# Kernel tuning notes

Measured on AMD Instinct MI355X. Metric: run time of the kernel, lower is better.

Reference implementation:

```python
import jax, jax.numpy as jnp
import numpy as np

B, IN_DIM, OUT_DIM = 4096, 8192, 8192

# Each of the 16 gates op_i(a,b) is affine in (1, a, b, a*b).
# Rows: [const, coef_a, coef_b, coef_ab] for gate i = 0..15.
GATE_COEF = np.array([
    [0.,  0.,  0.,  0.],   # 0: zeros
    [0.,  0.,  0.,  1.],   # 1: a*b
    [0.,  1.,  0., -1.],   # 2: a - a*b
    [0.,  1.,  0.,  0.],   # 3: a
    [0.,  0.,  1., -1.],   # 4: b - a*b
    [0.,  0.,  1.,  0.],   # 5: b
    [0.,  1.,  1., -2.],   # 6: a + b - 2ab (xor)
    [0.,  1.,  1., -1.],   # 7: a + b - ab (or)
    [1., -1., -1.,  1.],   # 8: 1 - (a + b - ab)
    [1., -1., -1.,  2.],   # 9: 1 - (a + b - 2ab)
    [1.,  0., -1.,  0.],   # 10: 1 - b
    [1.,  0., -1.,  1.],   # 11: 1 - b + ab
    [1., -1.,  0.,  0.],   # 12: 1 - a
    [1., -1.,  0.,  1.],   # 13: 1 - a + ab
    [1.,  0.,  0., -1.],   # 14: 1 - ab
    [1.,  0.,  0.,  0.],   # 15: ones
], dtype=np.float32)


def setup_inputs() -> dict:
    key = jax.random.key(0)
    k1, k2, k3, k4 = jax.random.split(key, 4)
    x = jax.random.uniform(k1, (B, IN_DIM), dtype=jnp.float32)
    weights = jax.random.normal(k2, (OUT_DIM, 16), dtype=jnp.float32)
    idx0 = jax.random.randint(k3, (OUT_DIM,), 0, IN_DIM)
    idx1 = jax.random.randint(k4, (OUT_DIM,), 0, IN_DIM)
    return {"x": x, "weights": weights, "idx0": idx0, "idx1": idx1}


def reference(x, weights, idx0, idx1):
    # training path: soft mixture over 16 gates
    p = jax.nn.softmax(weights, axis=-1)          # [out_dim, 16]
    c = p @ jnp.asarray(GATE_COEF)                # [out_dim, 4]: sum_i p_i * op_i collapsed
    a = x[:, idx0]                                # [B, out_dim]
    b = x[:, idx1]                                # [B, out_dim]
    return c[:, 0] + c[:, 1] * a + c[:, 2] * b + c[:, 3] * (a * b)
```

## Files before the change

kernel.cpp:

```cpp
#include <hip/hip_runtime.h>

#define IN_DIM 8192
#define OUT_DIM 8192
#define NROWS 4096
#define THREADS 1024
#define GRID 256
#define RPB (NROWS / GRID)
#define JG (OUT_DIM / (THREADS * 4))

static_assert(GRID * RPB == NROWS, "row partition");
static_assert(JG * THREADS * 4 == OUT_DIM, "col partition");

typedef float v4f __attribute__((ext_vector_type(4)));

#define BLOCK_SYNC_LDS()                                   \
  do {                                                     \
    asm volatile("s_waitcnt lgkmcnt(0)" ::: "memory");     \
    __builtin_amdgcn_s_barrier();                          \
    asm volatile("" ::: "memory");                         \
  } while (0)

static __device__ __forceinline__ void softmax_c(const float* __restrict__ w, int jbase,
                                                 v4f* C0, v4f* C1, v4f* C2, v4f* C3) {
  static constexpr float G[16][4] = {
      {0.f, 0.f, 0.f, 0.f}, {0.f, 0.f, 0.f, 1.f}, {0.f, 1.f, 0.f, -1.f}, {0.f, 1.f, 0.f, 0.f},
      {0.f, 0.f, 1.f, -1.f}, {0.f, 0.f, 1.f, 0.f}, {0.f, 1.f, 1.f, -2.f}, {0.f, 1.f, 1.f, -1.f},
      {1.f, -1.f, -1.f, 1.f}, {1.f, -1.f, -1.f, 2.f}, {1.f, 0.f, -1.f, 0.f}, {1.f, 0.f, -1.f, 1.f},
      {1.f, -1.f, 0.f, 0.f}, {1.f, -1.f, 0.f, 1.f}, {1.f, 0.f, 0.f, -1.f}, {1.f, 0.f, 0.f, 0.f}};
#pragma unroll
  for (int q = 0; q < 4; ++q) {
    const float4* wp = (const float4*)(w + (size_t)(jbase + q) * 16);
    float4 w0 = wp[0], w1 = wp[1], w2 = wp[2], w3 = wp[3];
    float wa[16] = {w0.x, w0.y, w0.z, w0.w, w1.x, w1.y, w1.z, w1.w,
                    w2.x, w2.y, w2.z, w2.w, w3.x, w3.y, w3.z, w3.w};
    float m = wa[0];
#pragma unroll
    for (int k = 1; k < 16; ++k) m = fmaxf(m, wa[k]);
    float s = 0.f;
    float p[16];
#pragma unroll
    for (int k = 0; k < 16; ++k) { p[k] = __expf(wa[k] - m); s += p[k]; }
    const float inv = 1.f / s;
    float a0 = 0.f, a1 = 0.f, a2 = 0.f, a3 = 0.f;
#pragma unroll
    for (int k = 0; k < 16; ++k) {
      a0 = fmaf(p[k], G[k][0], a0);
      a1 = fmaf(p[k], G[k][1], a1);
      a2 = fmaf(p[k], G[k][2], a2);
      a3 = fmaf(p[k], G[k][3], a3);
    }
    (*C0)[q] = a0 * inv; (*C1)[q] = a1 * inv; (*C2)[q] = a2 * inv; (*C3)[q] = a3 * inv;
  }
}

__global__ __launch_bounds__(THREADS, 4) void gate_fused(
    const float* __restrict__ x, const float* __restrict__ w,
    const int* __restrict__ idx0, const int* __restrict__ idx1,
    float* __restrict__ out) {
  __shared__ __align__(16) float buf[2][IN_DIM];
  const int tid = threadIdx.x;
  const int r0 = blockIdx.x * RPB;

  int4 i0[JG], i1[JG];
  v4f C0[JG], C1[JG], C2[JG], C3[JG];
#pragma unroll
  for (int g = 0; g < JG; ++g) {
    const int j = tid * 4 + g * (THREADS * 4);
    i0[g] = *(const int4*)(idx0 + j);
    i1[g] = *(const int4*)(idx1 + j);
    softmax_c(w, j, &C0[g], &C1[g], &C2[g], &C3[g]);
  }

  v4f ra[2];
  const float* x0 = x + (size_t)r0 * IN_DIM;
#pragma unroll
  for (int t = 0; t < 2; ++t) ra[t] = __builtin_nontemporal_load((const v4f*)x0 + tid + t * THREADS);
#pragma unroll
  for (int t = 0; t < 2; ++t) ((v4f*)buf[0])[tid + t * THREADS] = ra[t];
#pragma unroll
  for (int t = 0; t < 2; ++t)
    ra[t] = __builtin_nontemporal_load((const v4f*)(x0 + IN_DIM) + tid + t * THREADS);
  BLOCK_SYNC_LDS();

#pragma unroll 1
  for (int p = 0; p < RPB; ++p) {
    if (p + 1 < RPB) {
      v4f* dst = (v4f*)buf[(p + 1) & 1];
#pragma unroll
      for (int t = 0; t < 2; ++t) dst[tid + t * THREADS] = ra[t];
    }
    if (p + 2 < RPB) {
      const float* xs = x + (size_t)(r0 + p + 2) * IN_DIM;
#pragma unroll
      for (int t = 0; t < 2; ++t)
        ra[t] = __builtin_nontemporal_load((const v4f*)xs + tid + t * THREADS);
    }
    const float* bufc = buf[p & 1];
    float* o = out + (size_t)(r0 + p) * OUT_DIM;
#pragma unroll
    for (int g = 0; g < JG; ++g) {
      const int4 ia = i0[g], ib = i1[g];
      v4f a, b;
      a.x = bufc[ia.x]; a.y = bufc[ia.y]; a.z = bufc[ia.z]; a.w = bufc[ia.w];
      b.x = bufc[ib.x]; b.y = bufc[ib.y]; b.z = bufc[ib.z]; b.w = bufc[ib.w];
      const v4f r = C0[g] + C1[g] * a + C2[g] * b + C3[g] * (a * b);
      __builtin_nontemporal_store(r, (v4f*)(o + tid * 4 + g * (THREADS * 4)));
    }
    BLOCK_SYNC_LDS();
  }
}

extern "C" void kernel_launch(void* const* d_in, const int* in_sizes, int n_in,
                              void* d_out, int out_size, void* d_ws, size_t ws_size,
                              hipStream_t stream) {
  const float* x = (const float*)d_in[0];
  const float* weights = (const float*)d_in[1];
  const int* idx0 = (const int*)d_in[2];
  const int* idx1 = (const int*)d_in[3];
  float* out = (float*)d_out;
  gate_fused<<<GRID, THREADS, 0, stream>>>(x, weights, idx0, idx1, out);
}
```

Before: 246.6 us.

## Precompute gate coefficients in separate kernel and halve block size

Moves the softmax-to-coefficient computation into a small preceding kernel that writes the four coefficient arrays to workspace. The main kernel now reloads those coefficients from global memory on every row instead of holding them in registers. Blocks shrink to 512 threads and the grid doubles to 512, so each block handles fewer rows with its double-buffered LDS staging. This aims to remove redundant per-block softmax work and raise occupancy, at the cost of an extra launch and repeated coefficient loads from cache.

```diff
diff --git a/kernel.cpp b/kernel.cpp
--- a/kernel.cpp
+++ b/kernel.cpp
@@ -3,13 +3,15 @@
 #define IN_DIM 8192
 #define OUT_DIM 8192
 #define NROWS 4096
-#define THREADS 1024
-#define GRID 256
+#define THREADS 512
+#define GRID 512
 #define RPB (NROWS / GRID)
 #define JG (OUT_DIM / (THREADS * 4))
+#define SV (IN_DIM / (THREADS * 4))
 
 static_assert(GRID * RPB == NROWS, "row partition");
 static_assert(JG * THREADS * 4 == OUT_DIM, "col partition");
+static_assert(SV * THREADS * 4 == IN_DIM, "stage partition");
 
 typedef float v4f __attribute__((ext_vector_type(4)));
 
@@ -20,41 +22,47 @@
     asm volatile("" ::: "memory");                         \
   } while (0)
 
-static __device__ __forceinline__ void softmax_c(const float* __restrict__ w, int jbase,
-                                                 v4f* C0, v4f* C1, v4f* C2, v4f* C3) {
-  static constexpr float G[16][4] = {
-      {0.f, 0.f, 0.f, 0.f}, {0.f, 0.f, 0.f, 1.f}, {0.f, 1.f, 0.f, -1.f}, {0.f, 1.f, 0.f, 0.f},
-      {0.f, 0.f, 1.f, -1.f}, {0.f, 0.f, 1.f, 0.f}, {0.f, 1.f, 1.f, -2.f}, {0.f, 1.f, 1.f, -1.f},
-      {1.f, -1.f, -1.f, 1.f}, {1.f, -1.f, -1.f, 2.f}, {1.f, 0.f, -1.f, 0.f}, {1.f, 0.f, -1.f, 1.f},
-      {1.f, -1.f, 0.f, 0.f}, {1.f, -1.f, 0.f, 1.f}, {1.f, 0.f, 0.f, -1.f}, {1.f, 0.f, 0.f, 0.f}};
+__device__ __constant__ float GATE_COEF[16][4] = {
+    {0.f, 0.f, 0.f, 0.f}, {0.f, 0.f, 0.f, 1.f}, {0.f, 1.f, 0.f, -1.f}, {0.f, 1.f, 0.f, 0.f},
+    {0.f, 0.f, 1.f, -1.f}, {0.f, 0.f, 1.f, 0.f}, {0.f, 1.f, 1.f, -2.f}, {0.f, 1.f, 1.f, -1.f},
+    {1.f, -1.f, -1.f, 1.f}, {1.f, -1.f, -1.f, 2.f}, {1.f, 0.f, -1.f, 0.f}, {1.f, 0.f, -1.f, 1.f},
+    {1.f, -1.f, 0.f, 0.f}, {1.f, -1.f, 0.f, 1.f}, {1.f, 0.f, 0.f, -1.f}, {1.f, 0.f, 0.f, 0.f}};
+
+__global__ __launch_bounds__(256) void compute_c_kernel(const float* __restrict__ w,
+                                                        float* __restrict__ cp) {
+  int j = blockIdx.x * blockDim.x + threadIdx.x;
+  if (j >= OUT_DIM) return;
+  const float4* wv = (const float4*)(w + (size_t)j * 16);
+  float4 w0 = wv[0], w1 = wv[1], w2 = wv[2], w3 = wv[3];
+  float wa[16] = {w0.x, w0.y, w0.z, w0.w, w1.x, w1.y, w1.z, w1.w,
+                  w2.x, w2.y, w2.z, w2.w, w3.x, w3.y, w3.z, w3.w};
+  float m = wa[0];
 #pragma unroll
-  for (int q = 0; q < 4; ++q) {
-    const float4* wp = (const float4*)(w + (size_t)(jbase + q) * 16);
-    float4 w0 = wp[0], w1 = wp[1], w2 = wp[2], w3 = wp[3];
-    float wa[16] = {w0.x, w0.y, w0.z, w0.w, w1.x, w1.y, w1.z, w1.w,
-                    w2.x, w2.y, w2.z, w2.w, w3.x, w3.y, w3.z, w3.w};
-    float m = wa[0];
+  for (int k = 1; k < 16; ++k) m = fmaxf(m, wa[k]);
+  float p[16];
+  float s = 0.f;
 #pragma unroll
-    for (int k = 1; k < 16; ++k) m = fmaxf(m, wa[k]);
-    float s = 0.f;
-    float p[16];
+  for (int k = 0; k < 16; ++k) {
+    p[k] = __expf(wa[k] - m);
+    s += p[k];
+  }
+  float inv = 1.f / s;
+  float c0 = 0.f, c1 = 0.f, c2 = 0.f, c3 = 0.f;
 #pragma unroll
-    for (int k = 0; k < 16; ++k) { p[k] = __expf(wa[k] - m); s += p[k]; }
-    const float inv = 1.f / s;
-    float a0 = 0.f, a1 = 0.f, a2 = 0.f, a3 = 0.f;
-#pragma unroll
-    for (int k = 0; k < 16; ++k) {
-      a0 = fmaf(p[k], G[k][0], a0);
-      a1 = fmaf(p[k], G[k][1], a1);
-      a2 = fmaf(p[k], G[k][2], a2);
-      a3 = fmaf(p[k], G[k][3], a3);
-    }
-    (*C0)[q] = a0 * inv; (*C1)[q] = a1 * inv; (*C2)[q] = a2 * inv; (*C3)[q] = a3 * inv;
+  for (int k = 0; k < 16; ++k) {
+    c0 = fmaf(p[k], GATE_COEF[k][0], c0);
+    c1 = fmaf(p[k], GATE_COEF[k][1], c1);
+    c2 = fmaf(p[k], GATE_COEF[k][2], c2);
+    c3 = fmaf(p[k], GATE_COEF[k][3], c3);
   }
+  cp[j] = c0 * inv;
+  cp[j + OUT_DIM] = c1 * inv;
+  cp[j + 2 * OUT_DIM] = c2 * inv;
+  cp[j + 3 * OUT_DIM] = c3 * inv;
 }
 
-__global__ __launch_bounds__(THREADS, 4) void gate_fused(
-    const float* __restrict__ x, const float* __restrict__ w,
+__global__ __launch_bounds__(THREADS, 4) void gate_persist(
+    const float* __restrict__ x, const float* __restrict__ cp,
     const int* __restrict__ idx0, const int* __restrict__ idx1,
     float* __restrict__ out) {
   __shared__ __align__(16) float buf[2][IN_DIM];
@@ -62,23 +70,27 @@
   const int r0 = blockIdx.x * RPB;
 
   int4 i0[JG], i1[JG];
-  v4f C0[JG], C1[JG], C2[JG], C3[JG];
 #pragma unroll
   for (int g = 0; g < JG; ++g) {
     const int j = tid * 4 + g * (THREADS * 4);
     i0[g] = *(const int4*)(idx0 + j);
     i1[g] = *(const int4*)(idx1 + j);
-    softmax_c(w, j, &C0[g], &C1[g], &C2[g], &C3[g]);
   }
 
-  v4f ra[2];
+  const float* c0p = cp;
+  const float* c1p = cp + OUT_DIM;
+  const float* c2p = cp + 2 * OUT_DIM;
+  const float* c3p = cp + 3 * OUT_DIM;
+
+  v4f ra[SV];
   const float* x0 = x + (size_t)r0 * IN_DIM;
 #pragma unroll
-  for (int t = 0; t < 2; ++t) ra[t] = __builtin_nontemporal_load((const v4f*)x0 + tid + t * THREADS);
+  for (int t = 0; t < SV; ++t)
+    ra[t] = __builtin_nontemporal_load((const v4f*)x0 + tid + t * THREADS);
 #pragma unroll
-  for (int t = 0; t < 2; ++t) ((v4f*)buf[0])[tid + t * THREADS] = ra[t];
+  for (int t = 0; t < SV; ++t) ((v4f*)buf[0])[tid + t * THREADS] = ra[t];
 #pragma unroll
-  for (int t = 0; t < 2; ++t)
+  for (int t = 0; t < SV; ++t)
     ra[t] = __builtin_nontemporal_load((const v4f*)(x0 + IN_DIM) + tid + t * THREADS);
   BLOCK_SYNC_LDS();
 
@@ -87,24 +99,29 @@
     if (p + 1 < RPB) {
       v4f* dst = (v4f*)buf[(p + 1) & 1];
 #pragma unroll
-      for (int t = 0; t < 2; ++t) dst[tid + t * THREADS] = ra[t];
+      for (int t = 0; t < SV; ++t) dst[tid + t * THREADS] = ra[t];
     }
     if (p + 2 < RPB) {
       const float* xs = x + (size_t)(r0 + p + 2) * IN_DIM;
 #pragma unroll
-      for (int t = 0; t < 2; ++t)
+      for (int t = 0; t < SV; ++t)
         ra[t] = __builtin_nontemporal_load((const v4f*)xs + tid + t * THREADS);
     }
     const float* bufc = buf[p & 1];
     float* o = out + (size_t)(r0 + p) * OUT_DIM;
 #pragma unroll
     for (int g = 0; g < JG; ++g) {
+      const int j = tid * 4 + g * (THREADS * 4);
+      const v4f c0v = *(const v4f*)(c0p + j);
+      const v4f c1v = *(const v4f*)(c1p + j);
+      const v4f c2v = *(const v4f*)(c2p + j);
+      const v4f c3v = *(const v4f*)(c3p + j);
       const int4 ia = i0[g], ib = i1[g];
       v4f a, b;
       a.x = bufc[ia.x]; a.y = bufc[ia.y]; a.z = bufc[ia.z]; a.w = bufc[ia.w];
       b.x = bufc[ib.x]; b.y = bufc[ib.y]; b.z = bufc[ib.z]; b.w = bufc[ib.w];
-      const v4f r = C0[g] + C1[g] * a + C2[g] * b + C3[g] * (a * b);
-      __builtin_nontemporal_store(r, (v4f*)(o + tid * 4 + g * (THREADS * 4)));
+      const v4f r = c0v + c1v * a + c2v * b + c3v * (a * b);
+      __builtin_nontemporal_store(r, (v4f*)(o + j));
     }
     BLOCK_SYNC_LDS();
   }
@@ -118,5 +135,8 @@
   const int* idx0 = (const int*)d_in[2];
   const int* idx1 = (const int*)d_in[3];
   float* out = (float*)d_out;
-  gate_fused<<<GRID, THREADS, 0, stream>>>(x, weights, idx0, idx1, out);
+  float* cp = (float*)d_ws;
+
+  compute_c_kernel<<<OUT_DIM / 256, 256, 0, stream>>>(weights, cp);
+  gate_persist<<<GRID, THREADS, 0, stream>>>(x, cp, idx0, idx1, out);
 }
```

After: 238.0 us. -3.5%, faster.
